# Kernel optimization log

Measured on AMD Instinct MI355X. Metric: run time of the kernel, lower is better.

## Reference

```python
import jax, jax.numpy as jnp
import numpy as np

D = 512      # input_size
BR = 4       # branching factor (fan-in per internal node)
DEPTH = 8    # leaf level index; levels 0..DEPTH, root at level 0
N_NODES = (BR ** (DEPTH + 1) - 1) // (BR - 1)  # 87381


def setup_inputs() -> dict:
    key = jax.random.key(0)
    k1, k2, k3 = jax.random.split(key, 3)
    vectors = jax.random.normal(k1, (N_NODES, D), dtype=jnp.float32)
    scale = 1.0 / np.sqrt(D)
    wl = jax.random.normal(k2, (D, D), dtype=jnp.float32) * scale
    wr = jax.random.normal(k3, (D, D), dtype=jnp.float32) * scale
    return {"vectors": vectors, "wl": wl, "wr": wr, "branching": BR, "depth": DEPTH}


def reference(vectors, wl, wr, branching, depth):
    """Levelized CBTree forward over a complete `branching`-ary tree.

    vectors: [N, D] BFS-ordered node vectors (level l starts at (B^l-1)/(B-1)).
    Per node: h = tanh(x + sum_i lc_i * (h_i @ wl.T) + rc_i * (h_i @ wr.T)).
    """
    B, L = int(branching), int(depth)
    d = vectors.shape[-1]
    if B > 1:
        ind = jnp.arange(1, B + 1, dtype=vectors.dtype)  # 1-based child index
        lc = (B - ind) / (B - 1)
        rc = (ind - 1) / (B - 1)
    else:
        lc = jnp.full((1,), 0.5, dtype=vectors.dtype)
        rc = lc
    offsets = [(B ** l - 1) // (B - 1) for l in range(L + 1)]
    # leaves contribute their raw vectors (child.vector, no transform at leaf)
    h = vectors[offsets[L]: offsets[L] + B ** L]
    for l in range(L - 1, -1, -1):
        n = B ** l
        x = vectors[offsets[l]: offsets[l] + n]          # [n, D]
        hc = h.reshape(n, B, d)                           # children of level l
        tl = jnp.einsum('nbd,ed->nbe', hc, wl)            # wl(h_i) (Linear: h @ W.T)
        tr = jnp.einsum('nbd,ed->nbe', hc, wr)
        agg = jnp.einsum('b,nbe->ne', lc, tl) + jnp.einsum('b,nbe->ne', rc, tr)
        h = jnp.tanh(x + agg)                             # [n, D]
    return h  # [1, D] root hidden state
```

## Files before the change

### kernel.cpp

```cpp
#include <hip/hip_runtime.h>

typedef short short8 __attribute__((ext_vector_type(8)));
typedef float f32x4 __attribute__((ext_vector_type(4)));

#define D 512
#define KDIM 1024

static __device__ __forceinline__ unsigned short f2b(float f) {
    unsigned u = __builtin_bit_cast(unsigned, f);
    unsigned r = (u + 0x7fffu + ((u >> 16) & 1u)) >> 16;
    return (unsigned short)r;
}
static __device__ __forceinline__ float b2f(unsigned short u) {
    return __builtin_bit_cast(float, ((unsigned)u) << 16);
}
static __device__ __forceinline__ void split(float v, unsigned short& hi, unsigned short& lo) {
    hi = f2b(v);
    lo = f2b(v - b2f(hi));
}

static __device__ __forceinline__ void g2lds(const void* g, void* l) {
    __builtin_amdgcn_global_load_lds(
        (const __attribute__((address_space(1))) unsigned int*)g,
        (__attribute__((address_space(3))) unsigned int*)l, 16, 0, 0);
}

__global__ void pre_kernel(const float* __restrict__ leaves,
                           const float* __restrict__ wl, const float* __restrict__ wr,
                           unsigned short* __restrict__ Ah7,
                           unsigned short* __restrict__ Wh, unsigned short* __restrict__ Wl,
                           unsigned short* __restrict__ zbase) {
    int b = blockIdx.x;
    if (b < 4096) {
        int t = b * 256 + threadIdx.x;
        int p = t >> 6;
        int kc = (t & 63) << 3;
        const float c13 = 1.0f / 3.0f, c23 = 2.0f / 3.0f;
        const float* child = leaves;
        float4 a0 = *reinterpret_cast<const float4*>(child + (size_t)(4 * p + 0) * D + kc);
        float4 a1 = *reinterpret_cast<const float4*>(child + (size_t)(4 * p + 0) * D + kc + 4);
        float4 b0 = *reinterpret_cast<const float4*>(child + (size_t)(4 * p + 1) * D + kc);
        float4 b1 = *reinterpret_cast<const float4*>(child + (size_t)(4 * p + 1) * D + kc + 4);
        float4 c0 = *reinterpret_cast<const float4*>(child + (size_t)(4 * p + 2) * D + kc);
        float4 c1 = *reinterpret_cast<const float4*>(child + (size_t)(4 * p + 2) * D + kc + 4);
        float4 d0 = *reinterpret_cast<const float4*>(child + (size_t)(4 * p + 3) * D + kc);
        float4 d1 = *reinterpret_cast<const float4*>(child + (size_t)(4 * p + 3) * D + kc + 4);
        float ca[8] = {a0.x, a0.y, a0.z, a0.w, a1.x, a1.y, a1.z, a1.w};
        float cb[8] = {b0.x, b0.y, b0.z, b0.w, b1.x, b1.y, b1.z, b1.w};
        float cc[8] = {c0.x, c0.y, c0.z, c0.w, c1.x, c1.y, c1.z, c1.w};
        float cd[8] = {d0.x, d0.y, d0.z, d0.w, d1.x, d1.y, d1.z, d1.w};
        short8 uh, vh;
#pragma unroll
        for (int j = 0; j < 8; ++j) {
            float u = ca[j] + c23 * cb[j] + c13 * cc[j];
            float v = c13 * cb[j] + c23 * cc[j] + cd[j];
            uh[j] = (short)f2b(u);
            vh[j] = (short)f2b(v);
        }
        *reinterpret_cast<short8*>(&Ah7[(size_t)p * KDIM + kc]) = uh;
        *reinterpret_cast<short8*>(&Ah7[(size_t)p * KDIM + 512 + kc]) = vh;
    } else if (b < 6144) {
        int t = (b - 4096) * 256 + threadIdx.x;
        int e = t >> 10, k = t & 1023;
        float v = (k < 512) ? wl[e * 512 + k] : wr[e * 512 + (k - 512)];
        unsigned short h, l;
        split(v, h, l);
        Wh[t] = h; Wl[t] = l;
    } else {
        int t = (b - 6144) * 256 + threadIdx.x;
        *reinterpret_cast<short8*>(zbase + (size_t)t * 8) = (short8)0;
    }
}

__global__ __launch_bounds__(256)
void gemm_l7(const unsigned short* __restrict__ Ah, const unsigned short* __restrict__ Wh,
             const float* __restrict__ x, unsigned short* __restrict__ nAh, int n) {
    __shared__ __align__(16) unsigned short Ahs[128][64];
    __shared__ __align__(16) unsigned short Bhs[128][64];
    const int m0 = blockIdx.x * 128;
    const int e0 = blockIdx.y * 128;
    const int tid = threadIdx.x;
    const int lane = tid & 63, wid = tid >> 6;
    const int wr = (wid >> 1) * 64;
    const int wc = (wid & 1) * 64;

    f32x4 acc[4][4];
#pragma unroll
    for (int m = 0; m < 4; ++m)
#pragma unroll
        for (int nn = 0; nn < 4; ++nn) acc[m][nn] = (f32x4){0.f, 0.f, 0.f, 0.f};

    const int lrow = lane >> 3;
    const int lcol = (lane & 7) << 3;

    for (int kb = 0; kb < KDIM; kb += 64) {
#pragma unroll
        for (int p = 0; p < 4; ++p) {
            int row = p * 32 + wid * 8;
            g2lds(&Ah[(size_t)(m0 + row + lrow) * KDIM + kb + lcol], &Ahs[row][0]);
            g2lds(&Wh[(size_t)(e0 + row + lrow) * KDIM + kb + lcol], &Bhs[row][0]);
        }
        __syncthreads();
#pragma unroll
        for (int kk = 0; kk < 64; kk += 32) {
            const int ka = kk + ((lane >> 4) << 3);
            short8 af[4], bf[4];
#pragma unroll
            for (int m = 0; m < 4; ++m)
                af[m] = *reinterpret_cast<const short8*>(&Ahs[wr + m * 16 + (lane & 15)][ka]);
#pragma unroll
            for (int nn = 0; nn < 4; ++nn)
                bf[nn] = *reinterpret_cast<const short8*>(&Bhs[wc + nn * 16 + (lane & 15)][ka]);
#pragma unroll
            for (int m = 0; m < 4; ++m)
#pragma unroll
                for (int nn = 0; nn < 4; ++nn)
                    acc[m][nn] = __builtin_amdgcn_mfma_f32_16x16x32_bf16(af[m], bf[nn], acc[m][nn], 0, 0, 0);
        }
        __syncthreads();
    }

    const int dr = (lane >> 4) << 2;
    const int dc = lane & 15;
    const float c13 = 1.0f / 3.0f, c23 = 2.0f / 3.0f;
#pragma unroll
    for (int m = 0; m < 4; ++m) {
        int rbase = m0 + wr + m * 16 + dr;
        if (rbase >= n) continue;
#pragma unroll
        for (int nn = 0; nn < 4; ++nn) {
            int col = e0 + wc + nn * 16 + dc;
            float hv[4];
#pragma unroll
            for (int j = 0; j < 4; ++j) {
                int row = rbase + j;
                hv[j] = (row < n) ? tanhf(acc[m][nn][j] + x[(size_t)row * D + col]) : 0.f;
            }
            int p = rbase >> 2;
            float u = hv[0] + c23 * hv[1] + c13 * hv[2];
            float v = c13 * hv[1] + c23 * hv[2] + hv[3];
            nAh[(size_t)p * KDIM + col] = f2b(u);
            nAh[(size_t)p * KDIM + 512 + col] = f2b(v);
        }
    }
}

#define MBUF 4
__global__ __launch_bounds__(256)
void gemm_mid(const unsigned short* __restrict__ Ah, const unsigned short* __restrict__ Wh,
              const float* __restrict__ x,
              unsigned short* __restrict__ nAh, unsigned short* __restrict__ nAl, int n) {
    __shared__ __align__(16) unsigned short AhS[MBUF][64][64];
    __shared__ __align__(16) unsigned short BhS[MBUF][128][64];
    const int m0 = blockIdx.x * 64;
    const int e0 = blockIdx.y * 128;
    const int tid = threadIdx.x;
    const int lane = tid & 63, wid = tid >> 6;
    const int wm = (wid >> 1) * 32;
    const int wc = (wid & 1) * 64;
    const int lrow = lane >> 3, lcol = (lane & 7) << 3;

    auto stage = [&](int s) {
        int slot = s & 3;
        int kb = s * 64;
#pragma unroll
        for (int p = 0; p < 2; ++p) {
            int row = wid * 16 + p * 8;
            g2lds(&Ah[(size_t)(m0 + row + lrow) * KDIM + kb + lcol], &AhS[slot][row][0]);
        }
#pragma unroll
        for (int p = 0; p < 4; ++p) {
            int row = wid * 32 + p * 8;
            g2lds(&Wh[(size_t)(e0 + row + lrow) * KDIM + kb + lcol], &BhS[slot][row][0]);
        }
    };

    f32x4 acc[2][4];
#pragma unroll
    for (int m = 0; m < 2; ++m)
#pragma unroll
        for (int nn = 0; nn < 4; ++nn) acc[m][nn] = (f32x4){0.f, 0.f, 0.f, 0.f};

    stage(0); stage(1); stage(2);

#pragma unroll
    for (int t = 0; t < 16; ++t) {
        if (t <= 13)      { asm volatile("s_waitcnt vmcnt(12)" ::: "memory"); }
        else if (t == 14) { asm volatile("s_waitcnt vmcnt(6)"  ::: "memory"); }
        else              { asm volatile("s_waitcnt vmcnt(0)"  ::: "memory"); }
        __builtin_amdgcn_sched_barrier(0);
        __builtin_amdgcn_s_barrier();
        __builtin_amdgcn_sched_barrier(0);
        if (t + 3 < 16) stage(t + 3);
        const int slot = t & 3;
#pragma unroll
        for (int kk = 0; kk < 64; kk += 32) {
            const int ka = kk + ((lane >> 4) << 3);
            short8 af[2], bf[4];
#pragma unroll
            for (int m = 0; m < 2; ++m)
                af[m] = *reinterpret_cast<const short8*>(&AhS[slot][wm + m * 16 + (lane & 15)][ka]);
#pragma unroll
            for (int nn = 0; nn < 4; ++nn)
                bf[nn] = *reinterpret_cast<const short8*>(&BhS[slot][wc + nn * 16 + (lane & 15)][ka]);
#pragma unroll
            for (int m = 0; m < 2; ++m)
#pragma unroll
                for (int nn = 0; nn < 4; ++nn)
                    acc[m][nn] = __builtin_amdgcn_mfma_f32_16x16x32_bf16(af[m], bf[nn], acc[m][nn], 0, 0, 0);
        }
    }

    const int dr = (lane >> 4) << 2;
    const int dc = lane & 15;
    const float c13 = 1.0f / 3.0f, c23 = 2.0f / 3.0f;
#pragma unroll
    for (int m = 0; m < 2; ++m) {
        int rbase = m0 + wm + m * 16 + dr;
        if (rbase >= n) continue;
#pragma unroll
        for (int nn = 0; nn < 4; ++nn) {
            int col = e0 + wc + nn * 16 + dc;
            float hv[4];
#pragma unroll
            for (int j = 0; j < 4; ++j) {
                int row = rbase + j;
                hv[j] = (row < n) ? tanhf(acc[m][nn][j] + x[(size_t)row * D + col]) : 0.f;
            }
            int p = rbase >> 2;
            float u = hv[0] + c23 * hv[1] + c13 * hv[2];
            float v = c13 * hv[1] + c23 * hv[2] + hv[3];
            unsigned short h_, l_;
            split(u, h_, l_);
            nAh[(size_t)p * KDIM + col] = h_;
            nAl[(size_t)p * KDIM + col] = l_;
            split(v, h_, l_);
            nAh[(size_t)p * KDIM + 512 + col] = h_;
            nAl[(size_t)p * KDIM + 512 + col] = l_;
        }
    }
}

#define TBUF 6
template <bool FINAL>
__global__ __launch_bounds__(256)
void gemm_tiny(const unsigned short* __restrict__ Ah, const unsigned short* __restrict__ Al,
               const unsigned short* __restrict__ Wh, const unsigned short* __restrict__ Wl,
               const float* __restrict__ x,
               unsigned short* __restrict__ nAh, unsigned short* __restrict__ nAl,
               float* __restrict__ out, int n) {
    __shared__ __align__(16) unsigned short AhS[TBUF][32][64];
    __shared__ __align__(16) unsigned short AlS[TBUF][32][64];
    __shared__ __align__(16) unsigned short BhS[TBUF][64][64];
    __shared__ __align__(16) unsigned short BlS[TBUF][64][64];
    const int m0 = blockIdx.x * 32;
    const int e0 = blockIdx.y * 64;
    const int tid = threadIdx.x;
    const int lane = tid & 63, wid = tid >> 6;
    const int lrow = lane >> 3, lcol = (lane & 7) << 3;

    auto stage = [&](int s) {
        int slot = s % TBUF;
        int kb = s * 64;
        {
            int row = wid * 8;
            size_t g = (size_t)(m0 + row + lrow) * KDIM + kb + lcol;
            g2lds(&Ah[g], &AhS[slot][row][0]);
            g2lds(&Al[g], &AlS[slot][row][0]);
        }
#pragma unroll
        for (int p = 0; p < 2; ++p) {
            int row = wid * 16 + p * 8;
            size_t g = (size_t)(e0 + row + lrow) * KDIM + kb + lcol;
            g2lds(&Wh[g], &BhS[slot][row][0]);
            g2lds(&Wl[g], &BlS[slot][row][0]);
        }
    };

    f32x4 acc[2];
    acc[0] = (f32x4){0.f, 0.f, 0.f, 0.f};
    acc[1] = (f32x4){0.f, 0.f, 0.f, 0.f};

    stage(0); stage(1); stage(2); stage(3); stage(4);

#pragma unroll
    for (int t = 0; t < 16; ++t) {
        if (t <= 11)      { asm volatile("s_waitcnt vmcnt(24)" ::: "memory"); }
        else if (t == 12) { asm volatile("s_waitcnt vmcnt(18)" ::: "memory"); }
        else if (t == 13) { asm volatile("s_waitcnt vmcnt(12)" ::: "memory"); }
        else if (t == 14) { asm volatile("s_waitcnt vmcnt(6)"  ::: "memory"); }
        else              { asm volatile("s_waitcnt vmcnt(0)"  ::: "memory"); }
        __builtin_amdgcn_sched_barrier(0);
        __builtin_amdgcn_s_barrier();
        __builtin_amdgcn_sched_barrier(0);
        if (t + 5 < 16) stage(t + 5);
        const int slot = t % TBUF;
#pragma unroll
        for (int kk = 0; kk < 64; kk += 32) {
            const int ka = kk + ((lane >> 4) << 3);
            short8 afh[2], afl[2], bh, bl;
#pragma unroll
            for (int m = 0; m < 2; ++m) {
                afh[m] = *reinterpret_cast<const short8*>(&AhS[slot][m * 16 + (lane & 15)][ka]);
                afl[m] = *reinterpret_cast<const short8*>(&AlS[slot][m * 16 + (lane & 15)][ka]);
            }
            bh = *reinterpret_cast<const short8*>(&BhS[slot][wid * 16 + (lane & 15)][ka]);
            bl = *reinterpret_cast<const short8*>(&BlS[slot][wid * 16 + (lane & 15)][ka]);
#pragma unroll
            for (int m = 0; m < 2; ++m) {
                acc[m] = __builtin_amdgcn_mfma_f32_16x16x32_bf16(afh[m], bh, acc[m], 0, 0, 0);
                acc[m] = __builtin_amdgcn_mfma_f32_16x16x32_bf16(afh[m], bl, acc[m], 0, 0, 0);
                acc[m] = __builtin_amdgcn_mfma_f32_16x16x32_bf16(afl[m], bh, acc[m], 0, 0, 0);
            }
        }
    }

    const int dr = (lane >> 4) << 2;
    const int dc = lane & 15;
    const float c13 = 1.0f / 3.0f, c23 = 2.0f / 3.0f;
#pragma unroll
    for (int m = 0; m < 2; ++m) {
        int rbase = m0 + m * 16 + dr;
        if (rbase >= n) continue;
        int col = e0 + wid * 16 + dc;
        float hv[4];
#pragma unroll
        for (int j = 0; j < 4; ++j) {
            int row = rbase + j;
            hv[j] = (row < n) ? tanhf(acc[m][j] + x[(size_t)row * D + col]) : 0.f;
        }
        if (FINAL) {
            if (rbase == 0) out[col] = hv[0];
        } else {
            int p = rbase >> 2;
            float u = hv[0] + c23 * hv[1] + c13 * hv[2];
            float v = c13 * hv[1] + c23 * hv[2] + hv[3];
            unsigned short h_, l_;
            split(u, h_, l_);
            nAh[(size_t)p * KDIM + col] = h_;
            nAl[(size_t)p * KDIM + col] = l_;
            split(v, h_, l_);
            nAh[(size_t)p * KDIM + 512 + col] = h_;
            nAl[(size_t)p * KDIM + 512 + col] = l_;
        }
    }
}

extern "C" void kernel_launch(void* const* d_in, const int* in_sizes, int n_in,
                              void* d_out, int out_size, void* d_ws, size_t ws_size,
                              hipStream_t stream) {
    const float* vectors = (const float*)d_in[0];
    const float* wl = (const float*)d_in[1];
    const float* wr = (const float*)d_in[2];
    float* out = (float*)d_out;
    char* ws = (char*)d_ws;

    size_t cur = 0;
    auto alloc = [&](size_t bytes) -> char* {
        char* p = ws + cur;
        cur += (bytes + 255) & ~(size_t)255;
        return p;
    };
    unsigned short* Wh = (unsigned short*)alloc((size_t)512 * 1024 * 2);
    unsigned short* Wl = (unsigned short*)alloc((size_t)512 * 1024 * 2);
    const int arows[8] = {32, 32, 32, 64, 256, 1024, 4096, 16384};
    unsigned short *Ah[8], *Al[8];
    for (int l = 7; l >= 0; --l) {
        Ah[l] = (unsigned short*)alloc((size_t)arows[l] * KDIM * 2);
        Al[l] = (unsigned short*)alloc((size_t)arows[l] * KDIM * 2);
    }

    size_t off8 = 0;
    { size_t o = 0, c = 1; for (int l = 0; l <= 8; ++l) { if (l == 8) off8 = o; o += c; c *= 4; } }
    size_t off7 = off8 - 16384;

    pre_kernel<<<6240, 256, 0, stream>>>(vectors + off8 * (size_t)D, wl, wr,
                                         Ah[7], Wh, Wl, Ah[2]);

    gemm_l7<<<dim3(128, 4), 256, 0, stream>>>(
        Ah[7], Wh, vectors + off7 * (size_t)D, Ah[6], 16384);

    gemm_mid<<<dim3(64, 4), 256, 0, stream>>>(
        Ah[6], Wh, vectors + (off7 - 4096) * (size_t)D, Ah[5], Al[5], 4096);

    const int xo[6] = {0, 1, 5, 21, 85, 341};
    for (int l = 5; l >= 1; --l) {
        int n = 1 << (2 * l);
        int gx = (n + 31) / 32;
        gemm_tiny<false><<<dim3(gx, 8), 256, 0, stream>>>(
            Ah[l], Al[l], Wh, Wl, vectors + (size_t)xo[l] * D,
            Ah[l - 1], Al[l - 1], nullptr, n);
    }
    gemm_tiny<true><<<dim3(1, 8), 256, 0, stream>>>(
        Ah[0], Al[0], Wh, Wl, vectors, nullptr, nullptr, out, 1);
}
```

Measured before the change: 189.7 us.

## Double-buffer level-7 GEMM loads and widen tiny-GEMM K stages

The large level-7 GEMM now uses two LDS buffers with async global-to-LDS prefetch two stages ahead and explicit vmcnt waits, replacing the load-sync-compute-sync loop. This lets memory loads overlap with MFMA work. The tiny split-precision GEMM moves from 6 buffers of 64-wide K chunks to 3 buffers of 128-wide chunks, halving the number of barriers and stages but shortening the prefetch distance. The hand-tuned vmcnt counts must match the number of loads issued per stage, or results will be wrong.

```diff
diff --git a/kernel.cpp b/kernel.cpp
--- a/kernel.cpp
+++ b/kernel.cpp
@@ -75,49 +75,64 @@
 __global__ __launch_bounds__(256)
 void gemm_l7(const unsigned short* __restrict__ Ah, const unsigned short* __restrict__ Wh,
              const float* __restrict__ x, unsigned short* __restrict__ nAh, int n) {
-    __shared__ __align__(16) unsigned short Ahs[128][64];
-    __shared__ __align__(16) unsigned short Bhs[128][64];
+    __shared__ __align__(16) unsigned short AhS[2][128][64];
+    __shared__ __align__(16) unsigned short BhS[2][128][64];
     const int m0 = blockIdx.x * 128;
     const int e0 = blockIdx.y * 128;
     const int tid = threadIdx.x;
     const int lane = tid & 63, wid = tid >> 6;
     const int wr = (wid >> 1) * 64;
     const int wc = (wid & 1) * 64;
-
-    f32x4 acc[4][4];
-#pragma unroll
-    for (int m = 0; m < 4; ++m)
-#pragma unroll
-        for (int nn = 0; nn < 4; ++nn) acc[m][nn] = (f32x4){0.f, 0.f, 0.f, 0.f};
-
     const int lrow = lane >> 3;
     const int lcol = (lane & 7) << 3;
 
-    for (int kb = 0; kb < KDIM; kb += 64) {
+    auto stage = [&](int s) {
+        int slot = s & 1;
+        int kb = s * 64;
 #pragma unroll
         for (int p = 0; p < 4; ++p) {
             int row = p * 32 + wid * 8;
-            g2lds(&Ah[(size_t)(m0 + row + lrow) * KDIM + kb + lcol], &Ahs[row][0]);
-            g2lds(&Wh[(size_t)(e0 + row + lrow) * KDIM + kb + lcol], &Bhs[row][0]);
-        }
-        __syncthreads();
+            g2lds(&Ah[(size_t)(m0 + row + lrow) * KDIM + kb + lcol], &AhS[slot][row][0]);
+            g2lds(&Wh[(size_t)(e0 + row + lrow) * KDIM + kb + lcol], &BhS[slot][row][0]);
+        }
+    };
+
+    f32x4 acc[4][4];
+#pragma unroll
+    for (int m = 0; m < 4; ++m)
+#pragma unroll
+        for (int nn = 0; nn < 4; ++nn) acc[m][nn] = (f32x4){0.f, 0.f, 0.f, 0.f};
+
+    stage(0); stage(1);
+
+#pragma unroll
+    for (int t = 0; t < 16; ++t) {
+        if (t < 15) { asm volatile("s_waitcnt vmcnt(8)" ::: "memory"); }
+        else        { asm volatile("s_waitcnt vmcnt(0)" ::: "memory"); }
+        __builtin_amdgcn_sched_barrier(0);
+        __builtin_amdgcn_s_barrier();
+        __builtin_amdgcn_sched_barrier(0);
+        const int slot = t & 1;
 #pragma unroll
         for (int kk = 0; kk < 64; kk += 32) {
             const int ka = kk + ((lane >> 4) << 3);
             short8 af[4], bf[4];
 #pragma unroll
             for (int m = 0; m < 4; ++m)
-                af[m] = *reinterpret_cast<const short8*>(&Ahs[wr + m * 16 + (lane & 15)][ka]);
+                af[m] = *reinterpret_cast<const short8*>(&AhS[slot][wr + m * 16 + (lane & 15)][ka]);
 #pragma unroll
             for (int nn = 0; nn < 4; ++nn)
-                bf[nn] = *reinterpret_cast<const short8*>(&Bhs[wc + nn * 16 + (lane & 15)][ka]);
+                bf[nn] = *reinterpret_cast<const short8*>(&BhS[slot][wc + nn * 16 + (lane & 15)][ka]);
 #pragma unroll
             for (int m = 0; m < 4; ++m)
 #pragma unroll
                 for (int nn = 0; nn < 4; ++nn)
                     acc[m][nn] = __builtin_amdgcn_mfma_f32_16x16x32_bf16(af[m], bf[nn], acc[m][nn], 0, 0, 0);
         }
-        __syncthreads();
+        __builtin_amdgcn_sched_barrier(0);
+        __builtin_amdgcn_s_barrier();
+        __builtin_amdgcn_sched_barrier(0);
+        if (t + 2 < 16) stage(t + 2);
     }
 
     const int dr = (lane >> 4) << 2;
@@ -241,7 +256,7 @@
     }
 }
 
-#define TBUF 6
+#define TBUF 3
 template <bool FINAL>
 __global__ __launch_bounds__(256)
 void gemm_tiny(const unsigned short* __restrict__ Ah, const unsigned short* __restrict__ Al,
@@ -249,28 +264,30 @@
                const float* __restrict__ x,
                unsigned short* __restrict__ nAh, unsigned short* __restrict__ nAl,
                float* __restrict__ out, int n) {
-    __shared__ __align__(16) unsigned short AhS[TBUF][32][64];
-    __shared__ __align__(16) unsigned short AlS[TBUF][32][64];
-    __shared__ __align__(16) unsigned short BhS[TBUF][64][64];
-    __shared__ __align__(16) unsigned short BlS[TBUF][64][64];
+    __shared__ __align__(16) unsigned short AhS[TBUF][32][128];
+    __shared__ __align__(16) unsigned short AlS[TBUF][32][128];
+    __shared__ __align__(16) unsigned short BhS[TBUF][64][128];
+    __shared__ __align__(16) unsigned short BlS[TBUF][64][128];
     const int m0 = blockIdx.x * 32;
     const int e0 = blockIdx.y * 64;
     const int tid = threadIdx.x;
     const int lane = tid & 63, wid = tid >> 6;
-    const int lrow = lane >> 3, lcol = (lane & 7) << 3;
+    const int lrow = lane >> 4;
+    const int lcol = (lane & 15) << 3;
 
     auto stage = [&](int s) {
         int slot = s % TBUF;
-        int kb = s * 64;
-        {
-            int row = wid * 8;
+        int kb = s * 128;
+#pragma unroll
+        for (int p = 0; p < 2; ++p) {
+            int row = wid * 8 + p * 4;
             size_t g = (size_t)(m0 + row + lrow) * KDIM + kb + lcol;
             g2lds(&Ah[g], &AhS[slot][row][0]);
             g2lds(&Al[g], &AlS[slot][row][0]);
         }
 #pragma unroll
-        for (int p = 0; p < 2; ++p) {
-            int row = wid * 16 + p * 8;
+        for (int p = 0; p < 4; ++p) {
+            int row = wid * 16 + p * 4;
             size_t g = (size_t)(e0 + row + lrow) * KDIM + kb + lcol;
             g2lds(&Wh[g], &BhS[slot][row][0]);
             g2lds(&Wl[g], &BlS[slot][row][0]);
@@ -281,22 +298,19 @@
     acc[0] = (f32x4){0.f, 0.f, 0.f, 0.f};
     acc[1] = (f32x4){0.f, 0.f, 0.f, 0.f};
 
-    stage(0); stage(1); stage(2); stage(3); stage(4);
-
-#pragma unroll
-    for (int t = 0; t < 16; ++t) {
-        if (t <= 11)      { asm volatile("s_waitcnt vmcnt(24)" ::: "memory"); }
-        else if (t == 12) { asm volatile("s_waitcnt vmcnt(18)" ::: "memory"); }
-        else if (t == 13) { asm volatile("s_waitcnt vmcnt(12)" ::: "memory"); }
-        else if (t == 14) { asm volatile("s_waitcnt vmcnt(6)"  ::: "memory"); }
-        else              { asm volatile("s_waitcnt vmcnt(0)"  ::: "memory"); }
+    stage(0); stage(1);
+
+#pragma unroll
+    for (int t = 0; t < 8; ++t) {
+        if (t < 7) { asm volatile("s_waitcnt vmcnt(12)" ::: "memory"); }
+        else       { asm volatile("s_waitcnt vmcnt(0)"  ::: "memory"); }
         __builtin_amdgcn_sched_barrier(0);
         __builtin_amdgcn_s_barrier();
         __builtin_amdgcn_sched_barrier(0);
-        if (t + 5 < 16) stage(t + 5);
+        if (t + 2 < 8) stage(t + 2);
         const int slot = t % TBUF;
 #pragma unroll
-        for (int kk = 0; kk < 64; kk += 32) {
+        for (int kk = 0; kk < 128; kk += 32) {
             const int ka = kk + ((lane >> 4) << 3);
             short8 afh[2], afl[2], bh, bl;
 #pragma unroll
```

Measured after the change: 212.4 us. 12.0% more time.
